# Performance work log

Hardware: AMD Instinct MI355X
Metric: run time of the kernel (lower is better)

## Reference

```python
import jax, jax.numpy as jnp
import numpy as np

DIM, D_STATE, D_CONV, EXPAND = 1024, 16, 4, 2
D_INNER = EXPAND * DIM
DT_RANK = (DIM + 15) // 16  # 64
B, L = 2, 1024


def setup_inputs() -> dict:
    key = jax.random.key(0)
    ks = jax.random.split(key, 12)
    s = lambda k, shp, sc: jax.random.normal(k, shp, jnp.float32) * sc
    return {
        "x": s(ks[0], (B, L, DIM), 1.0),
        "ln_g": jnp.ones((DIM,), jnp.float32),
        "ln_b": jnp.zeros((DIM,), jnp.float32),
        "W_in": s(ks[1], (DIM, 2 * D_INNER), DIM ** -0.5),
        "conv_w": s(ks[2], (D_INNER, D_CONV), D_CONV ** -0.5),
        "conv_b": jnp.zeros((D_INNER,), jnp.float32),
        "W_x": s(ks[3], (D_INNER, DT_RANK + 2 * D_STATE), D_INNER ** -0.5),
        "W_dt": s(ks[4], (DT_RANK, D_INNER), DT_RANK ** -0.5),
        "b_dt": s(ks[5], (D_INNER,), 0.1),
        "A_log": jnp.log(jnp.broadcast_to(jnp.arange(1, D_STATE + 1, dtype=jnp.float32), (D_INNER, D_STATE))),
        "D_skip": jnp.ones((D_INNER,), jnp.float32),
        "W_out": s(ks[6], (D_INNER, DIM), D_INNER ** -0.5),
    }


def _mamba_block(x, ln_g, ln_b, W_in, conv_w, conv_b, W_x, W_dt, b_dt, A_log, D_skip, W_out):
    # LayerNorm over feature dim
    mu = jnp.mean(x, -1, keepdims=True)
    var = jnp.mean(jnp.square(x - mu), -1, keepdims=True)
    xn = (x - mu) * jax.lax.rsqrt(var + 1e-5) * ln_g + ln_b

    # in_proj -> (u, z), each (B, L, E)
    u, z = jnp.split(xn @ W_in, 2, axis=-1)

    # causal depthwise conv1d over L (kernel D_CONV) + SiLU
    up = jnp.pad(u, ((0, 0), (D_CONV - 1, 0), (0, 0)))
    uc = conv_b
    for k in range(D_CONV):
        uc = uc + conv_w[:, k] * up[:, k:k + L, :]
    uc = jax.nn.silu(uc)

    # input-dependent dt, B, C
    dbl = uc @ W_x
    dt = jax.nn.softplus(dbl[..., :DT_RANK] @ W_dt + b_dt)      # (B,L,E)
    Bc = dbl[..., DT_RANK:DT_RANK + D_STATE]                    # (B,L,N)
    Cc = dbl[..., DT_RANK + D_STATE:]                           # (B,L,N)

    A = -jnp.exp(A_log)                                         # (E,N)
    dA = jnp.exp(dt[..., None] * A)                             # (B,L,E,N)
    dBu = (dt * uc)[..., None] * Bc[:, :, None, :]              # (B,L,E,N)

    # selective scan: h_t = dA_t * h_{t-1} + dBu_t  (associative)
    def comb(c1, c2):
        a1, b1 = c1
        a2, b2 = c2
        return a2 * a1, a2 * b1 + b2

    _, h = jax.lax.associative_scan(comb, (dA, dBu), axis=1)

    y = jnp.einsum('blen,bln->ble', h, Cc) + uc * D_skip
    y = y * jax.nn.silu(z)
    return y @ W_out                                            # (B,L,DIM)


def reference(x, ln_g, ln_b, W_in, conv_w, conv_b, W_x, W_dt, b_dt, A_log, D_skip, W_out):
    return _mamba_block(x, ln_g, ln_b, W_in, conv_w, conv_b, W_x, W_dt, b_dt, A_log, D_skip, W_out)
```

## Files before the change

### kernel.cpp

```cpp
#include <hip/hip_runtime.h>
#include <hip/hip_bf16.h>

typedef __attribute__((ext_vector_type(4))) float  f32x4;
typedef __attribute__((ext_vector_type(8))) __bf16 bf16x8;

typedef __attribute__((address_space(1))) void gvoid_t;
typedef __attribute__((address_space(3))) void lvoid_t;

__device__ __forceinline__ void gld16(const void* g, void* l) {
    __builtin_amdgcn_global_load_lds((const gvoid_t*)g, (lvoid_t*)l, 16, 0, 0);
}

template <int N> __device__ __forceinline__ void vwait() {
    if constexpr (N == 0)      asm volatile("s_waitcnt vmcnt(0)" ::: "memory");
    else if constexpr (N == 6) asm volatile("s_waitcnt vmcnt(6)" ::: "memory");
    else if constexpr (N == 8) asm volatile("s_waitcnt vmcnt(8)" ::: "memory");
}

__device__ __forceinline__ unsigned short f2bf(float f) {
    unsigned u = __builtin_bit_cast(unsigned, f);
    u += 0x7fffu + ((u >> 16) & 1u);
    return (unsigned short)(u >> 16);
}
__device__ __forceinline__ float bf2f(unsigned short u) {
    return __builtin_bit_cast(float, (unsigned)u << 16);
}
__device__ __forceinline__ float silu(float x) {
    return x / (1.f + __expf(-x));
}

__device__ __forceinline__ void powers16(float p, float* dA) {
    float p2 = p * p, p4 = p2 * p2, p8 = p4 * p4, p16 = p8 * p8;
    float q[5] = {p, p2, p4, p8, p16};
    #pragma unroll
    for (int n = 0; n < 16; ++n) {
        int m = n + 1;
        float r = 1.f;
        bool first = true;
        #pragma unroll
        for (int bit = 0; bit < 5; ++bit) {
            if (m & (1 << bit)) {
                r = first ? q[bit] : r * q[bit];
                first = false;
            }
        }
        dA[n] = r;
    }
}

__device__ __forceinline__ void tr_cvt(const float* __restrict__ in,
                                       unsigned short* __restrict__ out,
                                       int K, int N, int Npad, int bnb, int bkb,
                                       float* sh) {
    float (*t)[33] = (float(*)[33])sh;
    int bn = bnb * 32, bk = bkb * 32;
    int c = threadIdx.x & 31, r0 = threadIdx.x >> 5;
    #pragma unroll
    for (int rr = r0; rr < 32; rr += 8) {
        int k = bk + rr, n = bn + c;
        t[rr][c] = (k < K && n < N) ? in[(size_t)k * N + n] : 0.f;
    }
    __syncthreads();
    #pragma unroll
    for (int rr = r0; rr < 32; rr += 8) {
        int n = bn + rr, k = bk + c;
        if (n < Npad && k < K) out[(size_t)n * K + k] = f2bf(t[c][rr]);
    }
}

__global__ __launch_bounds__(256) void k_prep(const float* __restrict__ x,
                                              const float* __restrict__ g,
                                              const float* __restrict__ b,
                                              unsigned short* __restrict__ xn,
                                              const float* __restrict__ W_in,  unsigned short* __restrict__ WIN_T,
                                              const float* __restrict__ W_out, unsigned short* __restrict__ WOUT_T,
                                              const float* __restrict__ W_dt,  unsigned short* __restrict__ WDT_T,
                                              const float* __restrict__ W_x,   unsigned short* __restrict__ WX_T) {
    __shared__ float sh[32 * 33];
    int bid = blockIdx.x;
    if (bid < 2048) {
        int row = bid;
        const float4* xr = (const float4*)(x + (size_t)row * 1024);
        float4 v = xr[threadIdx.x];
        float s  = v.x + v.y + v.z + v.w;
        float ss = v.x*v.x + v.y*v.y + v.z*v.z + v.w*v.w;
        #pragma unroll
        for (int o = 32; o > 0; o >>= 1) { s += __shfl_down(s, o); ss += __shfl_down(ss, o); }
        if ((threadIdx.x & 63) == 0) { sh[threadIdx.x >> 6] = s; sh[4 + (threadIdx.x >> 6)] = ss; }
        __syncthreads();
        s  = sh[0] + sh[1] + sh[2] + sh[3];
        ss = sh[4] + sh[5] + sh[6] + sh[7];
        float mu  = s * (1.f / 1024.f);
        float inv = rsqrtf(ss * (1.f / 1024.f) - mu * mu + 1e-5f);
        float4 gv = ((const float4*)g)[threadIdx.x];
        float4 bv = ((const float4*)b)[threadIdx.x];
        ushort4 o4;
        o4.x = f2bf((v.x - mu) * inv * gv.x + bv.x);
        o4.y = f2bf((v.y - mu) * inv * gv.y + bv.y);
        o4.z = f2bf((v.z - mu) * inv * gv.z + bv.z);
        o4.w = f2bf((v.w - mu) * inv * gv.w + bv.w);
        ((ushort4*)xn)[(size_t)row * 256 + threadIdx.x] = o4;
    } else if (bid < 6144) {
        int i = bid - 2048;  tr_cvt(W_in,  WIN_T,  1024, 4096, 4096, i & 127, i >> 7, sh);
    } else if (bid < 8192) {
        int i = bid - 6144;  tr_cvt(W_out, WOUT_T, 2048, 1024, 1024, i & 31,  i >> 5, sh);
    } else if (bid < 8320) {
        int i = bid - 8192;  tr_cvt(W_dt,  WDT_T,  64,   2048, 2048, i & 63,  i >> 6, sh);
    } else {
        int i = bid - 8320;  tr_cvt(W_x,   WX_T,   2048, 96,   128,  i & 3,   i >> 2, sh);
    }
}

template <int BM, int BN, int EPI>
__global__ __launch_bounds__(256) void k_gemm2(const unsigned short* __restrict__ A,
                                               const unsigned short* __restrict__ Bt,
                                               float* __restrict__ C,
                                               unsigned short* __restrict__ C2,
                                               unsigned short* __restrict__ C3,
                                               int kchunk, int lda, int ldb, int ldc,
                                               size_t zstride,
                                               const float* __restrict__ bias) {
    constexpr int PA = BM / 32, PB = BN / 32, NV = PA + PB;
    constexpr int MF = BM / 32, NF = BN / 32;
    __shared__ __attribute__((aligned(16))) unsigned short smA[2 * BM * 64];
    __shared__ __attribute__((aligned(16))) unsigned short smB[2 * BN * 64];

    int tid = threadIdx.x, wave = tid >> 6, lane = tid & 63;
    int bm = blockIdx.x * BM, bn = blockIdx.y * BN;
    int kstart = blockIdx.z * kchunk;
    int nt = kchunk >> 6;
    C += (size_t)blockIdx.z * zstride;
    int wm = (wave >> 1) * (BM / 2), wn = (wave & 1) * (BN / 2);
    int lr = lane & 15, lq = lane >> 4;
    int srow = wave * 8 + (lane >> 3);
    int scg  = lane & 7;

    f32x4 acc[MF][NF] = {};

    auto STAGE = [&](int buf, int k0) {
        unsigned short* dA = smA + buf * (BM * 64) + wave * 512;
        unsigned short* dB = smB + buf * (BN * 64) + wave * 512;
        #pragma unroll
        for (int p = 0; p < PA; ++p) {
            int row = p * 32 + srow;
            int gcol = ((scg ^ (row & 7)) << 3) + k0;
            gld16(A + (size_t)(bm + row) * lda + gcol, dA + p * 2048);
        }
        #pragma unroll
        for (int p = 0; p < PB; ++p) {
            int row = p * 32 + srow;
            int gcol = ((scg ^ (row & 7)) << 3) + k0;
            gld16(Bt + (size_t)(bn + row) * ldb + gcol, dB + p * 2048);
        }
    };

    STAGE(0, kstart);
    for (int t = 0; t < nt; ++t) {
        int cur = t & 1;
        if (t + 1 < nt) { STAGE(cur ^ 1, kstart + (t + 1) * 64); vwait<NV>(); }
        else            { vwait<0>(); }
        __builtin_amdgcn_s_barrier();
        const unsigned short* sA = smA + cur * (BM * 64);
        const unsigned short* sB = smB + cur * (BN * 64);
        #pragma unroll
        for (int ks = 0; ks < 2; ++ks) {
            int cg = (ks * 4 + lq) ^ (lr & 7);
            bf16x8 af[MF], bfv[NF];
            #pragma unroll
            for (int i = 0; i < MF; ++i)
                af[i] = *(const bf16x8*)(sA + (wm + i * 16 + lr) * 64 + (cg << 3));
            #pragma unroll
            for (int i = 0; i < NF; ++i)
                bfv[i] = *(const bf16x8*)(sB + (wn + i * 16 + lr) * 64 + (cg << 3));
            #pragma unroll
            for (int mi = 0; mi < MF; ++mi)
                #pragma unroll
                for (int ni = 0; ni < NF; ++ni)
                    acc[mi][ni] = __builtin_amdgcn_mfma_f32_16x16x32_bf16(af[mi], bfv[ni], acc[mi][ni], 0, 0, 0);
        }
        __builtin_amdgcn_s_barrier();
    }

    #pragma unroll
    for (int mi = 0; mi < MF; ++mi) {
        #pragma unroll
        for (int ni = 0; ni < NF; ++ni) {
            int c = bn + wn + ni * 16 + lr;
            #pragma unroll
            for (int v = 0; v < 4; ++v) {
                int r = bm + wm + mi * 16 + (lq << 2) + v;
                float val = acc[mi][ni][v];
                if (EPI == 0) {
                    C[(size_t)r * ldc + c] = val;
                } else if (EPI == 1) {
                    val += bias[c];
                    val = (val > 20.f) ? val : log1pf(__expf(val));
                    C[(size_t)r * ldc + c] = val;
                } else {
                    if (c < 2048) C2[(size_t)r * 2048 + c] = f2bf(val);
                    else          C3[(size_t)r * 2048 + (c - 2048)] = f2bf(silu(val));
                }
            }
        }
    }
}

__global__ __launch_bounds__(256) void k_red8(const float* __restrict__ part,
                                              float* __restrict__ dbl,
                                              unsigned short* __restrict__ dtr) {
    int idx = blockIdx.x * 256 + threadIdx.x;
    float s = 0.f;
    #pragma unroll
    for (int z = 0; z < 8; ++z) s += part[(size_t)z * 262144 + idx];
    dbl[idx] = s;
    int r = idx >> 7, c = idx & 127;
    if (c < 64) dtr[r * 64 + c] = f2bf(s);
}

__global__ __launch_bounds__(256) void k_conv2(const unsigned short* __restrict__ UB,
                                               const float* __restrict__ cw,
                                               const float* __restrict__ cb,
                                               unsigned short* __restrict__ ucb) {
    int idx = blockIdx.x * 256 + threadIdx.x;
    int e  = idx & 2047;
    int bl = idx >> 11;
    int l  = bl & 1023;
    float acc = cb[e];
    float4 wv = *(const float4*)(cw + e * 4);
    float w4[4] = {wv.x, wv.y, wv.z, wv.w};
    #pragma unroll
    for (int k = 0; k < 4; ++k) {
        int ls = l - 3 + k;
        if (ls >= 0) acc += w4[k] * bf2f(UB[(size_t)(bl - 3 + k) * 2048 + e]);
    }
    ucb[idx] = f2bf(silu(acc));
}


__global__ __launch_bounds__(256) void k_scan_p1(const unsigned short* __restrict__ ucb,
                                                 const float* __restrict__ dt,
                                                 const float* __restrict__ dbl,
                                                 const float* __restrict__ A_log,
                                                 float* __restrict__ aggH,
                                                 float* __restrict__ sdtb) {
    __shared__ float sB[32][16];
    int bid = blockIdx.x;
    int c = bid & 31, eblk = (bid >> 5) & 7, b = bid >> 8;
    int t = threadIdx.x;
    int e = eblk * 256 + t;
    int bl0 = b * 1024 + c * 32;
    if (t < 128) {
        int r = t >> 2, j4 = t & 3;
        *(float4*)&sB[r][j4 * 4] = *(const float4*)(dbl + (size_t)(bl0 + r) * 128 + 64 + j4 * 4);
    }
    __syncthreads();
    float Aen[16];
    #pragma unroll
    for (int n = 0; n < 16; ++n) Aen[n] = -__expf(A_log[e * 16 + n]);
    bool fastA = true;
    #pragma unroll
    for (int n = 1; n < 16; ++n)
        fastA = fastA && (fabsf(Aen[n] - (n + 1) * Aen[0]) <= 1e-3f);
    float h[16];
    #pragma unroll
    for (int n = 0; n < 16; ++n) h[n] = 0.f;
    float sdt = 0.f;
    size_t iu = (size_t)bl0 * 2048 + e;
    #pragma unroll 4
    for (int l = 0; l < 32; ++l) {
        float dtv = dt[iu];
        float ucv = bf2f(ucb[iu]);
        float dtu = dtv * ucv;
        float dA[16];
        if (fastA) {
            powers16(__expf(dtv * Aen[0]), dA);
        } else {
            #pragma unroll
            for (int n = 0; n < 16; ++n) dA[n] = __expf(dtv * Aen[n]);
        }
        #pragma unroll
        for (int n = 0; n < 16; ++n)
            h[n] = fmaf(dA[n], h[n], dtu * sB[l][n]);
        sdt += dtv;
        iu += 2048;
    }
    size_t o = ((size_t)(b * 32 + c) * 16) * 2048 + e;
    #pragma unroll
    for (int n = 0; n < 16; ++n) aggH[o + (size_t)n * 2048] = h[n];
    sdtb[(size_t)(b * 32 + c) * 2048 + e] = sdt;
}

__global__ __launch_bounds__(256) void k_scan_p2(const float* __restrict__ aggH,
                                                 const float* __restrict__ sdtb,
                                                 const float* __restrict__ A_log,
                                                 float* __restrict__ hinit) {
    int idx = blockIdx.x * 256 + threadIdx.x;
    int b = idx >> 15;
    int n = (idx >> 11) & 15;
    int e = idx & 2047;
    float Aen = -__expf(A_log[e * 16 + n]);
    float h = 0.f;
    #pragma unroll 4
    for (int c = 0; c < 32; ++c) {
        size_t base = ((size_t)(b * 32 + c) * 16 + n) * 2048 + e;
        hinit[base] = h;
        float a = __expf(sdtb[(size_t)(b * 32 + c) * 2048 + e] * Aen);
        h = fmaf(a, h, aggH[base]);
    }
}

__global__ __launch_bounds__(256) void k_scan_p3(const unsigned short* __restrict__ ucb,
                                                 const float* __restrict__ dt,
                                                 const float* __restrict__ dbl,
                                                 const unsigned short* __restrict__ sz,
                                                 const float* __restrict__ A_log,
                                                 const float* __restrict__ D_skip,
                                                 const float* __restrict__ hinit,
                                                 unsigned short* __restrict__ yg) {
    __shared__ float sBC[32][32];
    int bid = blockIdx.x;
    int c = bid & 31, eblk = (bid >> 5) & 7, b = bid >> 8;
    int t = threadIdx.x;
    int e = eblk * 256 + t;
    int bl0 = b * 1024 + c * 32;
    {
        int r = t >> 3, j = t & 7;
        *(float4*)&sBC[r][j * 4] = *(const float4*)(dbl + (size_t)(bl0 + r) * 128 + 64 + j * 4);
    }
    __syncthreads();
    float Aen[16];
    #pragma unroll
    for (int n = 0; n < 16; ++n) Aen[n] = -__expf(A_log[e * 16 + n]);
    bool fastA = true;
    #pragma unroll
    for (int n = 1; n < 16; ++n)
        fastA = fastA && (fabsf(Aen[n] - (n + 1) * Aen[0]) <= 1e-3f);
    float De = D_skip[e];
    size_t o = ((size_t)(b * 32 + c) * 16) * 2048 + e;
    float h[16];
    #pragma unroll
    for (int n = 0; n < 16; ++n) h[n] = hinit[o + (size_t)n * 2048];
    size_t iu = (size_t)bl0 * 2048 + e;
    #pragma unroll 4
    for (int l = 0; l < 32; ++l) {
        float dtv = dt[iu];
        float ucv = bf2f(ucb[iu]);
        float szv = bf2f(sz[iu]);
        float dtu = dtv * ucv;
        float dA[16];
        if (fastA) {
            powers16(__expf(dtv * Aen[0]), dA);
        } else {
            #pragma unroll
            for (int n = 0; n < 16; ++n) dA[n] = __expf(dtv * Aen[n]);
        }
        float y0 = 0.f, y1 = 0.f, y2 = 0.f, y3 = 0.f;
        #pragma unroll
        for (int n = 0; n < 16; n += 4) {
            h[n]     = fmaf(dA[n],     h[n],     dtu * sBC[l][n]);
            h[n + 1] = fmaf(dA[n + 1], h[n + 1], dtu * sBC[l][n + 1]);
            h[n + 2] = fmaf(dA[n + 2], h[n + 2], dtu * sBC[l][n + 2]);
            h[n + 3] = fmaf(dA[n + 3], h[n + 3], dtu * sBC[l][n + 3]);
            y0 = fmaf(h[n],     sBC[l][16 + n],     y0);
            y1 = fmaf(h[n + 1], sBC[l][16 + n + 1], y1);
            y2 = fmaf(h[n + 2], sBC[l][16 + n + 2], y2);
            y3 = fmaf(h[n + 3], sBC[l][16 + n + 3], y3);
        }
        float y = (y0 + y1) + (y2 + y3);
        y = (y + ucv * De) * szv;
        yg[iu] = f2bf(y);
        iu += 2048;
    }
}

extern "C" void kernel_launch(void* const* d_in, const int* in_sizes, int n_in,
                              void* d_out, int out_size, void* d_ws, size_t ws_size,
                              hipStream_t stream) {
    const float* x      = (const float*)d_in[0];
    const float* ln_g   = (const float*)d_in[1];
    const float* ln_b   = (const float*)d_in[2];
    const float* W_in   = (const float*)d_in[3];
    const float* conv_w = (const float*)d_in[4];
    const float* conv_b = (const float*)d_in[5];
    const float* W_x    = (const float*)d_in[6];
    const float* W_dt   = (const float*)d_in[7];
    const float* b_dt   = (const float*)d_in[8];
    const float* A_log  = (const float*)d_in[9];
    const float* D_skip = (const float*)d_in[10];
    const float* W_out  = (const float*)d_in[11];
    float* out = (float*)d_out;

    const size_t needed =
        (size_t)4096 * 1024 * 2 + (size_t)1024 * 2048 * 2 + (size_t)2048 * 64 * 2 +
        (size_t)128 * 2048 * 2 + (size_t)2048 * 1024 * 2 + (size_t)2048 * 4096 * 4 +
        (size_t)2048 * 2048 * 4 + (size_t)2048 * 2048 * 2 + (size_t)2048 * 128 * 4 +
        (size_t)2048 * 64 * 2 + (size_t)2048 * 2048 * 4 + (size_t)2048 * 2048 * 2;
    if (ws_size < needed) return;

    char* w = (char*)d_ws;
    unsigned short* WIN_T  = (unsigned short*)w; w += (size_t)4096 * 1024 * 2;
    unsigned short* WOUT_T = (unsigned short*)w; w += (size_t)1024 * 2048 * 2;
    unsigned short* WDT_T  = (unsigned short*)w; w += (size_t)2048 * 64 * 2;
    unsigned short* WX_T   = (unsigned short*)w; w += (size_t)128 * 2048 * 2;
    unsigned short* XN     = (unsigned short*)w; w += (size_t)2048 * 1024 * 2;
    unsigned short* UB     = (unsigned short*)w; w += (size_t)2048 * 2048 * 2;
    unsigned short* SZ     = (unsigned short*)w; w += (size_t)2048 * 2048 * 2;
    unsigned short* UCB    = (unsigned short*)w; w += (size_t)2048 * 2048 * 2;
    float*          DBL    = (float*)w;          w += (size_t)2048 * 128 * 4;
    unsigned short* DTR    = (unsigned short*)w; w += (size_t)2048 * 64 * 2;
    float*          DT     = (float*)w;          w += (size_t)2048 * 2048 * 4;
    unsigned short* YG     = (unsigned short*)w; w += (size_t)2048 * 2048 * 2;

    float* PART  = (float*)WIN_T;
    float* AGGH  = (float*)WIN_T;
    float* SDT   = (float*)XN;
    float* HINIT = (float*)UB;

    k_prep<<<8576, 256, 0, stream>>>(x, ln_g, ln_b, XN,
                                     W_in, WIN_T, W_out, WOUT_T, W_dt, WDT_T, W_x, WX_T);

    k_gemm2<128, 128, 2><<<dim3(16, 32, 1), 256, 0, stream>>>(XN, WIN_T, nullptr, UB, SZ, 1024, 1024, 1024, 2048, 0, nullptr);

    k_conv2<<<16384, 256, 0, stream>>>(UB, conv_w, conv_b, UCB);

    k_gemm2<64, 128, 0><<<dim3(32, 1, 8), 256, 0, stream>>>(UCB, WX_T, PART, nullptr, nullptr, 256, 2048, 2048, 128, (size_t)2048 * 128, nullptr);

    k_red8<<<1024, 256, 0, stream>>>(PART, DBL, DTR);

    k_gemm2<128, 128, 1><<<dim3(16, 16, 1), 256, 0, stream>>>(DTR, WDT_T, DT, nullptr, nullptr, 64, 64, 64, 2048, 0, b_dt);

    k_scan_p1<<<512, 256, 0, stream>>>(UCB, DT, DBL, A_log, AGGH, SDT);
    k_scan_p2<<<256, 256, 0, stream>>>(AGGH, SDT, A_log, HINIT);
    k_scan_p3<<<512, 256, 0, stream>>>(UCB, DT, DBL, SZ, A_log, D_skip, HINIT, YG);

    k_gemm2<64, 128, 0><<<dim3(32, 8, 1), 256, 0, stream>>>(YG, WOUT_T, out, nullptr, nullptr, 2048, 2048, 2048, 1024, 0, nullptr);
}
```

Before: 250.0 us.

## Fuse three-phase chunked scan into one cooperative kernel with grid syncs

Replaces the three scan kernels (chunk aggregate, cross-chunk prefix, chunk rescan) with one cooperative kernel that uses grid.sync between phases. It keeps the per-chunk dt and u values in shared memory so the third phase does not re-read them from global memory, and it removes two kernel launches. In exchange it depends on the cooperative launch succeeding (there is a fallback to the old path), and it adds about 50KB of LDS per block, which lowers occupancy. The grid barriers also add their own cost.

```diff
diff --git a/kernel.cpp b/kernel.cpp
--- a/kernel.cpp
+++ b/kernel.cpp
@@ -1,5 +1,8 @@
 #include <hip/hip_runtime.h>
 #include <hip/hip_bf16.h>
+#include <hip/hip_cooperative_groups.h>
+
+namespace cg = cooperative_groups;
 
 typedef __attribute__((ext_vector_type(4))) float  f32x4;
 typedef __attribute__((ext_vector_type(8))) __bf16 bf16x8;
@@ -236,6 +239,124 @@
     ucb[idx] = f2bf(silu(acc));
 }
 
+__global__ __launch_bounds__(256) void k_scan_fused(const unsigned short* __restrict__ ucb,
+                                                    const float* __restrict__ dt,
+                                                    const float* __restrict__ dbl,
+                                                    const unsigned short* __restrict__ sz,
+                                                    const float* __restrict__ A_log,
+                                                    const float* __restrict__ D_skip,
+                                                    float* __restrict__ aggH,
+                                                    float* __restrict__ sdtb,
+                                                    float* __restrict__ hinit,
+                                                    unsigned short* __restrict__ yg) {
+    cg::grid_group grid = cg::this_grid();
+    __shared__ float          sd[32][256];
+    __shared__ unsigned short su[32][256];
+    __shared__ float          sBC[32][32];
+
+    int bid = blockIdx.x;
+    int c = bid & 31, eblk = (bid >> 5) & 7, b = bid >> 8;
+    int t = threadIdx.x;
+    int e = eblk * 256 + t;
+    int bl0 = b * 1024 + c * 32;
+    {
+        int r = t >> 3, j = t & 7;
+        *(float4*)&sBC[r][j * 4] = *(const float4*)(dbl + (size_t)(bl0 + r) * 128 + 64 + j * 4);
+    }
+    float Aen[16];
+    #pragma unroll
+    for (int n = 0; n < 16; ++n) Aen[n] = -__expf(A_log[e * 16 + n]);
+    bool fastA = true;
+    #pragma unroll
+    for (int n = 1; n < 16; ++n)
+        fastA = fastA && (fabsf(Aen[n] - (n + 1) * Aen[0]) <= 1e-3f);
+    __syncthreads();
+
+    float h[16];
+    #pragma unroll
+    for (int n = 0; n < 16; ++n) h[n] = 0.f;
+    float sdt = 0.f;
+    size_t iu = (size_t)bl0 * 2048 + e;
+    #pragma unroll 4
+    for (int l = 0; l < 32; ++l) {
+        float dtv = dt[iu];
+        unsigned short uw = ucb[iu];
+        sd[l][t] = dtv;
+        su[l][t] = uw;
+        float dtu = dtv * bf2f(uw);
+        float dA[16];
+        if (fastA) {
+            powers16(__expf(dtv * Aen[0]), dA);
+        } else {
+            #pragma unroll
+            for (int n = 0; n < 16; ++n) dA[n] = __expf(dtv * Aen[n]);
+        }
+        #pragma unroll
+        for (int n = 0; n < 16; ++n)
+            h[n] = fmaf(dA[n], h[n], dtu * sBC[l][n]);
+        sdt += dtv;
+        iu += 2048;
+    }
+    size_t o = ((size_t)(b * 32 + c) * 16) * 2048 + e;
+    #pragma unroll
+    for (int n = 0; n < 16; ++n) aggH[o + (size_t)n * 2048] = h[n];
+    sdtb[(size_t)(b * 32 + c) * 2048 + e] = sdt;
+
+    grid.sync();
+
+    int gidx = bid * 256 + t;
+    if (gidx < 65536) {
+        int b2 = gidx >> 15;
+        int n2 = (gidx >> 11) & 15;
+        int e2 = gidx & 2047;
+        float Aen2 = -__expf(A_log[e2 * 16 + n2]);
+        float hh = 0.f;
+        #pragma unroll 4
+        for (int c2 = 0; c2 < 32; ++c2) {
+            size_t base = ((size_t)(b2 * 32 + c2) * 16 + n2) * 2048 + e2;
+            hinit[base] = hh;
+            float a = __expf(sdtb[(size_t)(b2 * 32 + c2) * 2048 + e2] * Aen2);
+            hh = fmaf(a, hh, aggH[base]);
+        }
+    }
+
+    grid.sync();
+
+    float De = D_skip[e];
+    #pragma unroll
+    for (int n = 0; n < 16; ++n) h[n] = hinit[o + (size_t)n * 2048];
+    iu = (size_t)bl0 * 2048 + e;
+    #pragma unroll 4
+    for (int l = 0; l < 32; ++l) {
+        float dtv = sd[l][t];
+        float ucv = bf2f(su[l][t]);
+        float szv = bf2f(sz[iu]);
+        float dtu = dtv * ucv;
+        float dA[16];
+        if (fastA) {
+            powers16(__expf(dtv * Aen[0]), dA);
+        } else {
+            #pragma unroll
+            for (int n = 0; n < 16; ++n) dA[n] = __expf(dtv * Aen[n]);
+        }
+        float y0 = 0.f, y1 = 0.f, y2 = 0.f, y3 = 0.f;
+        #pragma unroll
+        for (int n = 0; n < 16; n += 4) {
+            h[n]     = fmaf(dA[n],     h[n],     dtu * sBC[l][n]);
+            h[n + 1] = fmaf(dA[n + 1], h[n + 1], dtu * sBC[l][n + 1]);
+            h[n + 2] = fmaf(dA[n + 2], h[n + 2], dtu * sBC[l][n + 2]);
+            h[n + 3] = fmaf(dA[n + 3], h[n + 3], dtu * sBC[l][n + 3]);
+            y0 = fmaf(h[n],     sBC[l][16 + n],     y0);
+            y1 = fmaf(h[n + 1], sBC[l][16 + n + 1], y1);
+            y2 = fmaf(h[n + 2], sBC[l][16 + n + 2], y2);
+            y3 = fmaf(h[n + 3], sBC[l][16 + n + 3], y3);
+        }
+        float y = (y0 + y1) + (y2 + y3);
+        y = (y + ucv * De) * szv;
+        yg[iu] = f2bf(y);
+        iu += 2048;
+    }
+}
 
 __global__ __launch_bounds__(256) void k_scan_p1(const unsigned short* __restrict__ ucb,
                                                  const float* __restrict__ dt,
@@ -272,9 +393,8 @@
         float ucv = bf2f(ucb[iu]);
         float dtu = dtv * ucv;
         float dA[16];
-        if (fastA) {
-            powers16(__expf(dtv * Aen[0]), dA);
-        } else {
+        if (fastA) powers16(__expf(dtv * Aen[0]), dA);
+        else {
             #pragma unroll
             for (int n = 0; n < 16; ++n) dA[n] = __expf(dtv * Aen[n]);
         }
@@ -348,9 +468,8 @@
         float szv = bf2f(sz[iu]);
         float dtu = dtv * ucv;
         float dA[16];
-        if (fastA) {
-            powers16(__expf(dtv * Aen[0]), dA);
-        } else {
+        if (fastA) powers16(__expf(dtv * Aen[0]), dA);
+        else {
             #pragma unroll
             for (int n = 0; n < 16; ++n) dA[n] = __expf(dtv * Aen[n]);
         }
@@ -429,9 +548,28 @@
 
     k_gemm2<128, 128, 1><<<dim3(16, 16, 1), 256, 0, stream>>>(DTR, WDT_T, DT, nullptr, nullptr, 64, 64, 64, 2048, 0, b_dt);
 
-    k_scan_p1<<<512, 256, 0, stream>>>(UCB, DT, DBL, A_log, AGGH, SDT);
-    k_scan_p2<<<256, 256, 0, stream>>>(AGGH, SDT, A_log, HINIT);
-    k_scan_p3<<<512, 256, 0, stream>>>(UCB, DT, DBL, SZ, A_log, D_skip, HINIT, YG);
+    {
+        const unsigned short* a_ucb = UCB;
+        const float* a_dt = DT;
+        const float* a_dbl = DBL;
+        const unsigned short* a_sz = SZ;
+        const float* a_al = A_log;
+        const float* a_ds = D_skip;
+        float* a_aggH = AGGH;
+        float* a_sdt = SDT;
+        float* a_hinit = HINIT;
+        unsigned short* a_yg = YG;
+        void* args[] = {&a_ucb, &a_dt, &a_dbl, &a_sz, &a_al, &a_ds,
+                        &a_aggH, &a_sdt, &a_hinit, &a_yg};
+        hipError_t err = hipLaunchCooperativeKernel((const void*)k_scan_fused,
+                                                    dim3(512), dim3(256),
+                                                    args, 0, stream);
+        if (err != hipSuccess) {
+            k_scan_p1<<<512, 256, 0, stream>>>(UCB, DT, DBL, A_log, AGGH, SDT);
+            k_scan_p2<<<256, 256, 0, stream>>>(AGGH, SDT, A_log, HINIT);
+            k_scan_p3<<<512, 256, 0, stream>>>(UCB, DT, DBL, SZ, A_log, D_skip, HINIT, YG);
+        }
+    }
 
     k_gemm2<64, 128, 0><<<dim3(32, 8, 1), 256, 0, stream>>>(YG, WOUT_T, out, nullptr, nullptr, 2048, 2048, 2048, 1024, 0, nullptr);
 }
```

New measurement: 468.2 us. 87.3% more time.
